# Kernel tuning notes

Measured on AMD Instinct MI355X. Metric: run time of the kernel, lower is better.

## Reference

```python
import jax, jax.numpy as jnp
import numpy as np

N_NODES = 50000
N_IN = 512
HIDDEN = 64
N_CLASSES = 40
N_EDGES = 800000


def setup_inputs() -> dict:
    key = jax.random.key(0)
    ks = jax.random.split(key, 8)
    x = jax.random.normal(ks[0], (N_NODES, N_IN), dtype=jnp.float32)
    edge_index = jax.random.randint(ks[1], (2, N_EDGES), 0, N_NODES, dtype=jnp.int64)
    s1 = 1.0 / np.sqrt(N_IN)
    s2 = 1.0 / np.sqrt(HIDDEN)
    W1 = jax.random.uniform(ks[2], (N_IN, HIDDEN), jnp.float32, -s1, s1)
    b1 = jax.random.uniform(ks[3], (HIDDEN,), jnp.float32, -s1, s1)
    W2 = jax.random.uniform(ks[4], (HIDDEN, HIDDEN), jnp.float32, -s2, s2)
    b2 = jax.random.uniform(ks[5], (HIDDEN,), jnp.float32, -s2, s2)
    Wo = jax.random.uniform(ks[6], (HIDDEN, N_CLASSES), jnp.float32, -s2, s2)
    bo = jax.random.uniform(ks[7], (N_CLASSES,), jnp.float32, -s2, s2)
    return {"x": x, "W1": W1, "b1": b1, "W2": W2, "b2": b2,
            "Wo": Wo, "bo": bo, "edge_index": edge_index}


def _gcn_conv(x, W, b, row, col, n_nodes):
    # h = lin(x)
    h = x @ W + b
    # degree over row (with self loops already appended)
    deg = jnp.zeros((n_nodes,), dtype=h.dtype).at[row].add(1.0)
    dis = deg ** -0.5  # deg >= 1 thanks to self loops
    norm = dis[row] * dis[col]  # [E]
    # message: norm * x_j where x_j = h[row] (source); aggregate to col (target)
    msg = norm[:, None] * h[row]  # [E, d]
    return jax.ops.segment_sum(msg, col, num_segments=n_nodes)


def reference(x, W1, b1, W2, b2, Wo, bo, edge_index):
    n = x.shape[0]
    # add_self_loops
    loop = jnp.arange(n, dtype=edge_index.dtype)
    row = jnp.concatenate([edge_index[0], loop])
    col = jnp.concatenate([edge_index[1], loop])
    h = _gcn_conv(x, W1, b1, row, col, n)
    h = jax.nn.relu(h)
    # dropout is identity in eval mode (training=False)
    h = _gcn_conv(h, W2, b2, row, col, n)
    logits = h @ Wo + bo
    return jax.nn.log_softmax(logits, axis=1)
```

## Files before the change

kernel.cpp:

```cpp
#include <hip/hip_runtime.h>
#include <hip/hip_fp16.h>
#include <cstdint>

#define N_NODES   50000
#define N_IN      512
#define HIDDEN    64
#define N_CLASSES 40
#define N_EDGES   800000

#define G_BLOCKS  200
#define EPB       4000
#define NBINS     196
#define SCAN_N    (NBINS * G_BLOCKS)
#define SCAN_NB   ((SCAN_N + 1023) / 1024)
#define FOLD_N    (N_IN * 64 + 64 * 64 + 64)
#define FOLD_B    ((FOLD_N + 255) / 256)

#define OFF_HA    0u
#define OFF_HB    6400000u
#define OFF_DIS   12800000u
#define OFF_OFFS  13000000u
#define OFF_HISTC 13200016u
#define OFF_HISTR 13356816u
#define OFF_BSUM  13513616u
#define OFF_COLS  13514128u
#define OFF_ROWS  16714128u
#define OFF_EPACK 19914128u
#define OFF_W1T   23114128u
#define OFF_W2OT  23179664u
#define OFF_B2O   23187856u

typedef __attribute__((ext_vector_type(8))) short short8_t;
typedef __attribute__((ext_vector_type(4))) float f32x4;

__device__ __forceinline__ ushort f2bf(float f) {
    uint u = __float_as_uint(f);
    uint r = (u + 0x7FFFu + ((u >> 16) & 1u)) >> 16;
    return (ushort)r;
}
__device__ __forceinline__ float bf2f(ushort h) {
    return __uint_as_float((uint)h << 16);
}

__global__ __launch_bounds__(256) void hist_fold(const int* __restrict__ erow,
                                                 const int* __restrict__ ecol,
                                                 int* __restrict__ histC,
                                                 int* __restrict__ histR,
                                                 const float* __restrict__ W1,
                                                 const float* __restrict__ W2,
                                                 const float* __restrict__ Wo,
                                                 const float* __restrict__ b2,
                                                 ushort* __restrict__ w1t,
                                                 ushort* __restrict__ w2ot,
                                                 float* __restrict__ b2o) {
    __shared__ int hc[NBINS], hr[NBINS];
    int t = threadIdx.x;
    if (blockIdx.x < G_BLOCKS) {
        int b = blockIdx.x;
        if (t < NBINS) { hc[t] = 0; hr[t] = 0; }
        __syncthreads();
        int s = b * EPB;
        for (int i = s + t; i < s + EPB; i += 256) {
            atomicAdd(&hc[ecol[i] >> 8], 1);
            atomicAdd(&hr[erow[i] >> 8], 1);
        }
        __syncthreads();
        if (t < NBINS) {
            histC[t * G_BLOCKS + b] = hc[t];
            histR[t * G_BLOCKS + b] = hr[t];
        }
    } else {
        int i = (blockIdx.x - G_BLOCKS) * 256 + t;
        if (i < N_IN * 64) {
            int k = i >> 6, n = i & 63;
            w1t[n * N_IN + k] = f2bf(W1[i]);
        } else if (i < N_IN * 64 + 64 * 64) {
            int j = i - N_IN * 64;
            int k = j >> 6, n = j & 63;
            float v = 0.f;
            if (n < N_CLASSES)
                for (int jj = 0; jj < HIDDEN; jj++)
                    v += W2[k * HIDDEN + jj] * Wo[jj * N_CLASSES + n];
            w2ot[n * HIDDEN + k] = f2bf(v);
        } else if (i < FOLD_N) {
            int c = i - N_IN * 64 - 64 * 64;
            float v = 0.f;
            if (c < N_CLASSES)
                for (int jj = 0; jj < HIDDEN; jj++)
                    v += b2[jj] * Wo[jj * N_CLASSES + c];
            b2o[c] = v;
        }
    }
}

__global__ __launch_bounds__(256) void scan1(int* __restrict__ histC,
                                             int* __restrict__ histR,
                                             int* __restrict__ bsum, int n) {
    int* a  = blockIdx.y ? histR : histC;
    int* bs = bsum + blockIdx.y * 64;
    int t = threadIdx.x;
    int g = blockIdx.x * 1024 + t * 4;
    int v[4];
#pragma unroll
    for (int i = 0; i < 4; i++) v[i] = (g + i < n) ? a[g + i] : 0;
    int s = v[0] + v[1] + v[2] + v[3];
    int lane = t & 63, wid = t >> 6;
    int x = s;
#pragma unroll
    for (int d = 1; d < 64; d <<= 1) {
        int y = __shfl_up(x, d);
        if (lane >= d) x += y;
    }
    __shared__ int wt[4];
    if (lane == 63) wt[wid] = x;
    __syncthreads();
    int wo = 0;
    for (int w = 0; w < wid; w++) wo += wt[w];
    int run = wo + x - s;
#pragma unroll
    for (int i = 0; i < 4; i++) {
        if (g + i < n) a[g + i] = run;
        run += v[i];
    }
    if (t == 255) bs[blockIdx.x] = wo + x;
}

__global__ void scan2(int* bsum, int nb) {
    int* bs = bsum + blockIdx.x * 64;
    int lane = threadIdx.x;
    int v = (lane < nb) ? bs[lane] : 0;
    int x = v;
#pragma unroll
    for (int d = 1; d < 64; d <<= 1) {
        int y = __shfl_up(x, d);
        if (lane >= d) x += y;
    }
    if (lane < nb) bs[lane] = x - v;
}

__global__ __launch_bounds__(256) void scan3(int* __restrict__ histC,
                                             int* __restrict__ histR,
                                             const int* __restrict__ bsum, int n) {
    int* a = blockIdx.y ? histR : histC;
    const int* bs = bsum + blockIdx.y * 64;
    int i = blockIdx.x * 256 + threadIdx.x;
    if (i < n) a[i] += bs[i >> 10];
}

__global__ __launch_bounds__(256) void scatter_k(const int* __restrict__ erow,
                                                 const int* __restrict__ ecol,
                                                 const int* __restrict__ scC,
                                                 const int* __restrict__ scR,
                                                 uint* __restrict__ colSorted,
                                                 int* __restrict__ rowSorted) {
    __shared__ int curC[NBINS], curR[NBINS];
    int t = threadIdx.x, b = blockIdx.x;
    if (t < NBINS) {
        curC[t] = scC[t * G_BLOCKS + b];
        curR[t] = scR[t * G_BLOCKS + b];
    }
    __syncthreads();
    int s = b * EPB;
    for (int i = s + t; i < s + EPB; i += 256) {
        int r = erow[i], c = ecol[i];
        int p = atomicAdd(&curC[c >> 8], 1);
        colSorted[p] = (uint)r | ((uint)c << 16);
        int q = atomicAdd(&curR[r >> 8], 1);
        rowSorted[q] = r;
    }
}

__global__ __launch_bounds__(256) void fine_row(const int* __restrict__ rowSorted,
                                                const int* __restrict__ scR,
                                                float* __restrict__ disv) {
    __shared__ int cnt[256];
    int bin = blockIdx.x, t = threadIdx.x;
    int base = scR[bin * G_BLOCKS];
    int end  = (bin == NBINS - 1) ? N_EDGES : scR[(bin + 1) * G_BLOCKS];
    cnt[t] = 0;
    __syncthreads();
    for (int i = base + t; i < end; i += 256)
        atomicAdd(&cnt[rowSorted[i] & 255], 1);
    __syncthreads();
    int node = bin * 256 + t;
    if (node < N_NODES) disv[node] = rsqrtf((float)(cnt[t] + 1));
}

__global__ __launch_bounds__(256) void fine_col(const uint* __restrict__ colSorted,
                                                const int* __restrict__ scC,
                                                const float* __restrict__ disv,
                                                int* __restrict__ offs,
                                                uint* __restrict__ epack) {
    __shared__ int cnt[256];
    __shared__ int excl[256];
    __shared__ int wt[4];
    __shared__ float dvs[256];
    int bin = blockIdx.x, t = threadIdx.x;
    int base = scC[bin * G_BLOCKS];
    int end  = (bin == NBINS - 1) ? N_EDGES : scC[(bin + 1) * G_BLOCKS];
    cnt[t] = 0;
    int node = bin * 256 + t;
    dvs[t] = (node < N_NODES) ? disv[node] : 0.f;
    __syncthreads();
    for (int i = base + t; i < end; i += 256)
        atomicAdd(&cnt[(colSorted[i] >> 16) & 255], 1);
    __syncthreads();
    int lane = t & 63, w = t >> 6;
    int v = cnt[t];
    int x = v;
#pragma unroll
    for (int d = 1; d < 64; d <<= 1) {
        int y = __shfl_up(x, d);
        if (lane >= d) x += y;
    }
    if (lane == 63) wt[w] = x;
    __syncthreads();
    int wo = 0;
    for (int u = 0; u < w; u++) wo += wt[u];
    excl[t] = wo + x - v;
    cnt[t] = 0;
    if (node <= N_NODES) offs[node] = base + wo + x - v;
    __syncthreads();
    for (int i = base + t; i < end; i += 256) {
        uint pv = colSorted[i];
        int cl = (pv >> 16) & 255;
        int src = (int)(pv & 0xFFFFu);
        int p = base + excl[cl] + atomicAdd(&cnt[cl], 1);
        float nrm = disv[src] * dvs[cl];
        ushort nb_ = __half_as_ushort(__float2half_rn(nrm));
        epack[p] = ((uint)nb_ << 16) | (uint)src;
    }
}

template <bool ABF16>
__global__ __launch_bounds__(256) void gemm_mfma(const void* __restrict__ Av,
                                                 const ushort* __restrict__ WT,
                                                 const float* __restrict__ bias,
                                                 ushort* __restrict__ C,
                                                 int M, int K) {
    __shared__ ushort Asb[64][72];
    __shared__ ushort Bsb[64][72];
    int t = threadIdx.x;
    int w = t >> 6, lane = t & 63;
    int wm = w >> 1, wn = w & 1;
    int lr = lane & 15, lg = lane >> 4;
    int blockRow = blockIdx.x * 64;

    f32x4 acc[2][2];
#pragma unroll
    for (int i = 0; i < 2; i++)
#pragma unroll
        for (int j = 0; j < 2; j++) acc[i][j] = (f32x4){0.f, 0.f, 0.f, 0.f};

    for (int kk = 0; kk < K; kk += 64) {
#pragma unroll
        for (int u = 0; u < 2; u++) {
            int idx = t + u * 256;
            int m = idx >> 3;
            int k8 = (idx & 7) * 8;
            int row = blockRow + m;
            short8_t s;
            if (ABF16) {
                const ushort* A16 = (const ushort*)Av;
                if (row < M) s = *(const short8_t*)(A16 + (size_t)row * K + kk + k8);
                else s = (short8_t){0,0,0,0,0,0,0,0};
            } else {
                const float* A32 = (const float*)Av;
                float4 a0, a1;
                if (row < M) {
                    const float* p = A32 + (size_t)row * K + kk + k8;
                    a0 = *(const float4*)p;
                    a1 = *(const float4*)(p + 4);
                } else {
                    a0 = make_float4(0.f, 0.f, 0.f, 0.f);
                    a1 = a0;
                }
                s[0] = (short)f2bf(a0.x); s[1] = (short)f2bf(a0.y);
                s[2] = (short)f2bf(a0.z); s[3] = (short)f2bf(a0.w);
                s[4] = (short)f2bf(a1.x); s[5] = (short)f2bf(a1.y);
                s[6] = (short)f2bf(a1.z); s[7] = (short)f2bf(a1.w);
            }
            *(short8_t*)&Asb[m][k8] = s;
        }
#pragma unroll
        for (int u = 0; u < 2; u++) {
            int idx = t + u * 256;
            int n = idx >> 3;
            int k8 = (idx & 7) * 8;
            short8_t vv = *(const short8_t*)(WT + (size_t)n * K + kk + k8);
            *(short8_t*)&Bsb[n][k8] = vv;
        }
        __syncthreads();
#pragma unroll
        for (int ks = 0; ks < 2; ks++) {
            int k0 = ks * 32 + lg * 8;
            short8_t af[2], bf_[2];
#pragma unroll
            for (int mi = 0; mi < 2; mi++)
                af[mi] = *(const short8_t*)&Asb[wm * 32 + mi * 16 + lr][k0];
#pragma unroll
            for (int ni = 0; ni < 2; ni++)
                bf_[ni] = *(const short8_t*)&Bsb[wn * 32 + ni * 16 + lr][k0];
#pragma unroll
            for (int mi = 0; mi < 2; mi++)
#pragma unroll
                for (int ni = 0; ni < 2; ni++)
                    acc[mi][ni] = __builtin_amdgcn_mfma_f32_16x16x32_bf16(
                        af[mi], bf_[ni], acc[mi][ni], 0, 0, 0);
        }
        __syncthreads();
    }
#pragma unroll
    for (int mi = 0; mi < 2; mi++) {
#pragma unroll
        for (int ni = 0; ni < 2; ni++) {
            int col = wn * 32 + ni * 16 + lr;
            float bv = bias[col];
#pragma unroll
            for (int r = 0; r < 4; r++) {
                int row = blockRow + wm * 32 + mi * 16 + lg * 4 + r;
                if (row < M) C[(size_t)row * 64 + col] = f2bf(acc[mi][ni][r] + bv);
            }
        }
    }
}

template <int HEAD>
__global__ __launch_bounds__(256) void agg_v3(const ushort* __restrict__ H,
                                              const int* __restrict__ offs,
                                              const uint* __restrict__ epack,
                                              const float* __restrict__ disv,
                                              ushort* __restrict__ outH,
                                              const float* __restrict__ bo,
                                              float* __restrict__ outL) {
    int wv = (blockIdx.x * 256 + threadIdx.x) >> 6;
    int lane = threadIdx.x & 63;
    wv = __builtin_amdgcn_readfirstlane(wv);
    if (wv >= N_NODES) return;
    int s = offs[wv], e = offs[wv + 1];
    float dn = disv[wv];
    float acc = dn * dn *
        bf2f(__builtin_nontemporal_load(H + (size_t)wv * 64 + lane));

    int i = s;
    for (; i + 8 <= e; i += 8) {
        uint ep[8];
#pragma unroll
        for (int u = 0; u < 8; u++) ep[u] = epack[i + u];
        float hv[8];
#pragma unroll
        for (int u = 0; u < 8; u++)
            hv[u] = bf2f(__builtin_nontemporal_load(
                H + (size_t)(ep[u] & 0xFFFFu) * 64 + lane));
#pragma unroll
        for (int u = 0; u < 8; u++) {
            float w = __half2float(__ushort_as_half((ushort)(ep[u] >> 16)));
            acc = fmaf(w, hv[u], acc);
        }
    }
    if (i < e) {
        int cap = e - 1;
        uint ep[8];
#pragma unroll
        for (int u = 0; u < 8; u++) ep[u] = epack[min(i + u, cap)];
        float hv[8];
#pragma unroll
        for (int u = 0; u < 8; u++)
            hv[u] = bf2f(__builtin_nontemporal_load(
                H + (size_t)(ep[u] & 0xFFFFu) * 64 + lane));
#pragma unroll
        for (int u = 0; u < 8; u++) {
            uint wb = (i + u < e) ? (ep[u] >> 16) : 0u;
            float w = __half2float(__ushort_as_half((ushort)wb));
            acc = fmaf(w, hv[u], acc);
        }
    }

    if (!HEAD) {
        outH[(size_t)wv * 64 + lane] = f2bf(fmaxf(acc, 0.f));
    } else {
        float accL = (lane < N_CLASSES) ? acc + bo[lane] : -1e30f;
        float mx = accL;
#pragma unroll
        for (int d = 32; d; d >>= 1) mx = fmaxf(mx, __shfl_xor(mx, d));
        float ex = (lane < N_CLASSES) ? expf(accL - mx) : 0.f;
        float sm = ex;
#pragma unroll
        for (int d = 32; d; d >>= 1) sm += __shfl_xor(sm, d);
        if (lane < N_CLASSES)
            outL[(size_t)wv * N_CLASSES + lane] = accL - mx - logf(sm);
    }
}

extern "C" void kernel_launch(void* const* d_in, const int* in_sizes, int n_in,
                              void* d_out, int out_size, void* d_ws, size_t ws_size,
                              hipStream_t stream) {
    const float* x  = (const float*)d_in[0];
    const float* W1 = (const float*)d_in[1];
    const float* b1 = (const float*)d_in[2];
    const float* W2 = (const float*)d_in[3];
    const float* b2 = (const float*)d_in[4];
    const float* Wo = (const float*)d_in[5];
    const float* bo = (const float*)d_in[6];
    const int* ei   = (const int*)d_in[7];
    const int* erow = ei;
    const int* ecol = ei + N_EDGES;

    char* ws = (char*)d_ws;
    ushort* h_a   = (ushort*)(ws + OFF_HA);
    ushort* h_b   = (ushort*)(ws + OFF_HB);
    float* disv   = (float*)(ws + OFF_DIS);
    int*   offs   = (int*)(ws + OFF_OFFS);
    int*   histC  = (int*)(ws + OFF_HISTC);
    int*   histR  = (int*)(ws + OFF_HISTR);
    int*   bsum   = (int*)(ws + OFF_BSUM);
    uint*  colS   = (uint*)(ws + OFF_COLS);
    int*   rowS   = (int*)(ws + OFF_ROWS);
    uint*  epack  = (uint*)(ws + OFF_EPACK);
    ushort* w1t   = (ushort*)(ws + OFF_W1T);
    ushort* w2ot  = (ushort*)(ws + OFF_W2OT);
    float* b2o    = (float*)(ws + OFF_B2O);
    float* outp   = (float*)d_out;

    hist_fold<<<G_BLOCKS + FOLD_B, 256, 0, stream>>>(erow, ecol, histC, histR,
                                                     W1, W2, Wo, b2, w1t, w2ot, b2o);
    scan1<<<dim3(SCAN_NB, 2), 256, 0, stream>>>(histC, histR, bsum, SCAN_N);
    scan2<<<2, 64, 0, stream>>>(bsum, SCAN_NB);
    scan3<<<dim3((SCAN_N + 255) / 256, 2), 256, 0, stream>>>(histC, histR, bsum, SCAN_N);
    scatter_k<<<G_BLOCKS, 256, 0, stream>>>(erow, ecol, histC, histR, colS, rowS);
    fine_row<<<NBINS, 256, 0, stream>>>(rowS, histR, disv);
    fine_col<<<NBINS, 256, 0, stream>>>(colS, histC, disv, offs, epack);

    gemm_mfma<false><<<(N_NODES + 63) / 64, 256, 0, stream>>>(x, w1t, b1, h_a, N_NODES, N_IN);
    agg_v3<0><<<(N_NODES + 3) / 4, 256, 0, stream>>>(h_a, offs, epack, disv, h_b,
                                                     nullptr, nullptr);
    gemm_mfma<true><<<(N_NODES + 63) / 64, 256, 0, stream>>>(h_b, w2ot, b2o, h_a, N_NODES, HIDDEN);
    agg_v3<1><<<(N_NODES + 3) / 4, 256, 0, stream>>>(h_a, offs, epack, disv, nullptr,
                                                     bo, outp);
}
```

Baseline: 140.2 us.

## Fuse first GEMM with edge scatter and aggregate two edges per wave

The first dense GEMM now runs inside the edge-scatter kernel: separate blocks of one launch handle the GEMM and the scatter, so the two independent jobs overlap and one launch is dropped. The aggregation kernel splits each 64-lane wave into two halves. Each half reads a different neighbour edge with 32-bit loads of two bf16 features, and the halves are combined with a cross-half shuffle. This gives fewer load instructions and more edges in flight per wave, at the cost of a shuffle reduction and a reworked log-softmax that holds two classes per lane.

```diff
diff --git a/kernel.cpp b/kernel.cpp
--- a/kernel.cpp
+++ b/kernel.cpp
@@ -15,6 +15,7 @@
 #define SCAN_NB   ((SCAN_N + 1023) / 1024)
 #define FOLD_N    (N_IN * 64 + 64 * 64 + 64)
 #define FOLD_B    ((FOLD_N + 255) / 256)
+#define GEMM1_B   ((N_NODES + 63) / 64)
 
 #define OFF_HA    0u
 #define OFF_HB    6400000u
@@ -147,104 +148,17 @@
     if (i < n) a[i] += bs[i >> 10];
 }
 
-__global__ __launch_bounds__(256) void scatter_k(const int* __restrict__ erow,
-                                                 const int* __restrict__ ecol,
-                                                 const int* __restrict__ scC,
-                                                 const int* __restrict__ scR,
-                                                 uint* __restrict__ colSorted,
-                                                 int* __restrict__ rowSorted) {
-    __shared__ int curC[NBINS], curR[NBINS];
-    int t = threadIdx.x, b = blockIdx.x;
-    if (t < NBINS) {
-        curC[t] = scC[t * G_BLOCKS + b];
-        curR[t] = scR[t * G_BLOCKS + b];
-    }
-    __syncthreads();
-    int s = b * EPB;
-    for (int i = s + t; i < s + EPB; i += 256) {
-        int r = erow[i], c = ecol[i];
-        int p = atomicAdd(&curC[c >> 8], 1);
-        colSorted[p] = (uint)r | ((uint)c << 16);
-        int q = atomicAdd(&curR[r >> 8], 1);
-        rowSorted[q] = r;
-    }
-}
-
-__global__ __launch_bounds__(256) void fine_row(const int* __restrict__ rowSorted,
-                                                const int* __restrict__ scR,
-                                                float* __restrict__ disv) {
-    __shared__ int cnt[256];
-    int bin = blockIdx.x, t = threadIdx.x;
-    int base = scR[bin * G_BLOCKS];
-    int end  = (bin == NBINS - 1) ? N_EDGES : scR[(bin + 1) * G_BLOCKS];
-    cnt[t] = 0;
-    __syncthreads();
-    for (int i = base + t; i < end; i += 256)
-        atomicAdd(&cnt[rowSorted[i] & 255], 1);
-    __syncthreads();
-    int node = bin * 256 + t;
-    if (node < N_NODES) disv[node] = rsqrtf((float)(cnt[t] + 1));
-}
-
-__global__ __launch_bounds__(256) void fine_col(const uint* __restrict__ colSorted,
-                                                const int* __restrict__ scC,
-                                                const float* __restrict__ disv,
-                                                int* __restrict__ offs,
-                                                uint* __restrict__ epack) {
-    __shared__ int cnt[256];
-    __shared__ int excl[256];
-    __shared__ int wt[4];
-    __shared__ float dvs[256];
-    int bin = blockIdx.x, t = threadIdx.x;
-    int base = scC[bin * G_BLOCKS];
-    int end  = (bin == NBINS - 1) ? N_EDGES : scC[(bin + 1) * G_BLOCKS];
-    cnt[t] = 0;
-    int node = bin * 256 + t;
-    dvs[t] = (node < N_NODES) ? disv[node] : 0.f;
-    __syncthreads();
-    for (int i = base + t; i < end; i += 256)
-        atomicAdd(&cnt[(colSorted[i] >> 16) & 255], 1);
-    __syncthreads();
-    int lane = t & 63, w = t >> 6;
-    int v = cnt[t];
-    int x = v;
-#pragma unroll
-    for (int d = 1; d < 64; d <<= 1) {
-        int y = __shfl_up(x, d);
-        if (lane >= d) x += y;
-    }
-    if (lane == 63) wt[w] = x;
-    __syncthreads();
-    int wo = 0;
-    for (int u = 0; u < w; u++) wo += wt[u];
-    excl[t] = wo + x - v;
-    cnt[t] = 0;
-    if (node <= N_NODES) offs[node] = base + wo + x - v;
-    __syncthreads();
-    for (int i = base + t; i < end; i += 256) {
-        uint pv = colSorted[i];
-        int cl = (pv >> 16) & 255;
-        int src = (int)(pv & 0xFFFFu);
-        int p = base + excl[cl] + atomicAdd(&cnt[cl], 1);
-        float nrm = disv[src] * dvs[cl];
-        ushort nb_ = __half_as_ushort(__float2half_rn(nrm));
-        epack[p] = ((uint)nb_ << 16) | (uint)src;
-    }
-}
-
 template <bool ABF16>
-__global__ __launch_bounds__(256) void gemm_mfma(const void* __restrict__ Av,
-                                                 const ushort* __restrict__ WT,
-                                                 const float* __restrict__ bias,
-                                                 ushort* __restrict__ C,
-                                                 int M, int K) {
-    __shared__ ushort Asb[64][72];
-    __shared__ ushort Bsb[64][72];
+__device__ __forceinline__ void gemm_body(ushort (&Asb)[64][72], ushort (&Bsb)[64][72],
+                                          const void* __restrict__ Av,
+                                          const ushort* __restrict__ WT,
+                                          const float* __restrict__ bias,
+                                          ushort* __restrict__ C,
+                                          int M, int K, int blockRow) {
     int t = threadIdx.x;
     int w = t >> 6, lane = t & 63;
     int wm = w >> 1, wn = w & 1;
     int lr = lane & 15, lg = lane >> 4;
-    int blockRow = blockIdx.x * 64;
 
     f32x4 acc[2][2];
 #pragma unroll
@@ -325,8 +239,116 @@
     }
 }
 
+template <bool ABF16>
+__global__ __launch_bounds__(256) void gemm_mfma(const void* __restrict__ Av,
+                                                 const ushort* __restrict__ WT,
+                                                 const float* __restrict__ bias,
+                                                 ushort* __restrict__ C,
+                                                 int M, int K) {
+    __shared__ ushort Asb[64][72];
+    __shared__ ushort Bsb[64][72];
+    gemm_body<ABF16>(Asb, Bsb, Av, WT, bias, C, M, K, blockIdx.x * 64);
+}
+
+__global__ __launch_bounds__(256) void scatter_gemm(const float* __restrict__ x,
+                                                    const ushort* __restrict__ w1t,
+                                                    const float* __restrict__ b1,
+                                                    ushort* __restrict__ h_a,
+                                                    const int* __restrict__ erow,
+                                                    const int* __restrict__ ecol,
+                                                    const int* __restrict__ scC,
+                                                    const int* __restrict__ scR,
+                                                    uint* __restrict__ colSorted,
+                                                    int* __restrict__ rowSorted) {
+    __shared__ ushort Asb[64][72];
+    __shared__ ushort Bsb[64][72];
+    if (blockIdx.x < GEMM1_B) {
+        gemm_body<false>(Asb, Bsb, x, w1t, b1, h_a, N_NODES, N_IN, blockIdx.x * 64);
+        return;
+    }
+    int b = blockIdx.x - GEMM1_B;
+    int* curC = (int*)&Asb[0][0];
+    int* curR = curC + NBINS;
+    int t = threadIdx.x;
+    if (t < NBINS) {
+        curC[t] = scC[t * G_BLOCKS + b];
+        curR[t] = scR[t * G_BLOCKS + b];
+    }
+    __syncthreads();
+    int s = b * EPB;
+    for (int i = s + t; i < s + EPB; i += 256) {
+        int r = erow[i], c = ecol[i];
+        int p = atomicAdd(&curC[c >> 8], 1);
+        colSorted[p] = (uint)r | ((uint)c << 16);
+        int q = atomicAdd(&curR[r >> 8], 1);
+        rowSorted[q] = r;
+    }
+}
+
+__global__ __launch_bounds__(256) void fine_row(const int* __restrict__ rowSorted,
+                                                const int* __restrict__ scR,
+                                                float* __restrict__ disv) {
+    __shared__ int cnt[256];
+    int bin = blockIdx.x, t = threadIdx.x;
+    int base = scR[bin * G_BLOCKS];
+    int end  = (bin == NBINS - 1) ? N_EDGES : scR[(bin + 1) * G_BLOCKS];
+    cnt[t] = 0;
+    __syncthreads();
+    for (int i = base + t; i < end; i += 256)
+        atomicAdd(&cnt[rowSorted[i] & 255], 1);
+    __syncthreads();
+    int node = bin * 256 + t;
+    if (node < N_NODES) disv[node] = rsqrtf((float)(cnt[t] + 1));
+}
+
+__global__ __launch_bounds__(256) void fine_col(const uint* __restrict__ colSorted,
+                                                const int* __restrict__ scC,
+                                                const float* __restrict__ disv,
+                                                int* __restrict__ offs,
+                                                uint* __restrict__ epack) {
+    __shared__ int cnt[256];
+    __shared__ int excl[256];
+    __shared__ int wt[4];
+    __shared__ float dvs[256];
+    int bin = blockIdx.x, t = threadIdx.x;
+    int base = scC[bin * G_BLOCKS];
+    int end  = (bin == NBINS - 1) ? N_EDGES : scC[(bin + 1) * G_BLOCKS];
+    cnt[t] = 0;
+    int node = bin * 256 + t;
+    dvs[t] = (node < N_NODES) ? disv[node] : 0.f;
+    __syncthreads();
+    for (int i = base + t; i < end; i += 256)
+        atomicAdd(&cnt[(colSorted[i] >> 16) & 255], 1);
+    __syncthreads();
+    int lane = t & 63, w = t >> 6;
+    int v = cnt[t];
+    int x = v;
+#pragma unroll
+    for (int d = 1; d < 64; d <<= 1) {
+        int y = __shfl_up(x, d);
+        if (lane >= d) x += y;
+    }
+    if (lane == 63) wt[w] = x;
+    __syncthreads();
+    int wo = 0;
+    for (int u = 0; u < w; u++) wo += wt[u];
+    excl[t] = wo + x - v;
+    cnt[t] = 0;
+    if (node <= N_NODES) offs[node] = base + wo + x - v;
+    __syncthreads();
+    for (int i = base + t; i < end; i += 256) {
+        uint pv = colSorted[i];
+        int cl = (pv >> 16) & 255;
+        int src = (int)(pv & 0xFFFFu);
+        int p = base + excl[cl] + atomicAdd(&cnt[cl], 1);
+        float nrm = disv[src] * dvs[cl];
+        ushort nb_ = __half_as_ushort(__float2half_rn(nrm));
+        epack[p] = ((uint)nb_ << 16) | (uint)src;
+    }
+}
+
 template <int HEAD>
-__global__ __launch_bounds__(256) void agg_v3(const ushort* __restrict__ H,
+__global__ __launch_bounds__(256) void agg_v4(const ushort* __restrict__ H,
                                               const int* __restrict__ offs,
                                               const uint* __restrict__ epack,
                                               const float* __restrict__ disv,
@@ -337,25 +359,25 @@
     int lane = threadIdx.x & 63;
     wv = __builtin_amdgcn_readfirstlane(wv);
     if (wv >= N_NODES) return;
+    int c = lane & 31;
+    int g = lane >> 5;
     int s = offs[wv], e = offs[wv + 1];
     float dn = disv[wv];
-    float acc = dn * dn *
-        bf2f(__builtin_nontemporal_load(H + (size_t)wv * 64 + lane));
-
+    uint self = *(const uint*)(H + (size_t)wv * 64 + c * 2);
+
+    float acc0 = 0.f, acc1 = 0.f;
     int i = s;
     for (; i + 8 <= e; i += 8) {
         uint ep[8];
 #pragma unroll
         for (int u = 0; u < 8; u++) ep[u] = epack[i + u];
-        float hv[8];
-#pragma unroll
-        for (int u = 0; u < 8; u++)
-            hv[u] = bf2f(__builtin_nontemporal_load(
-                H + (size_t)(ep[u] & 0xFFFFu) * 64 + lane));
-#pragma unroll
-        for (int u = 0; u < 8; u++) {
-            float w = __half2float(__ushort_as_half((ushort)(ep[u] >> 16)));
-            acc = fmaf(w, hv[u], acc);
+#pragma unroll
+        for (int p = 0; p < 4; p++) {
+            uint eg = g ? ep[2 * p + 1] : ep[2 * p];
+            uint hv = *(const uint*)(H + (size_t)(eg & 0xFFFFu) * 64 + c * 2);
+            float w = __half2float(__ushort_as_half((ushort)(eg >> 16)));
+            acc0 = fmaf(w, bf2f((ushort)(hv & 0xFFFFu)), acc0);
+            acc1 = fmaf(w, bf2f((ushort)(hv >> 16)), acc1);
         }
     }
     if (i < e) {
@@ -363,32 +385,46 @@
         uint ep[8];
 #pragma unroll
         for (int u = 0; u < 8; u++) ep[u] = epack[min(i + u, cap)];
-        float hv[8];
-#pragma unroll
-        for (int u = 0; u < 8; u++)
-            hv[u] = bf2f(__builtin_nontemporal_load(
-                H + (size_t)(ep[u] & 0xFFFFu) * 64 + lane));
-#pragma unroll
-        for (int u = 0; u < 8; u++) {
-            uint wb = (i + u < e) ? (ep[u] >> 16) : 0u;
-            float w = __half2float(__ushort_as_half((ushort)wb));
-            acc = fmaf(w, hv[u], acc);
-        }
-    }
+#pragma unroll
+        for (int p = 0; p < 4; p++) {
+            int idx = i + 2 * p + g;
+            uint eg = g ? ep[2 * p + 1] : ep[2 * p];
+            uint hv = *(const uint*)(H + (size_t)(eg & 0xFFFFu) * 64 + c * 2);
+            float w = (idx < e)
+                ? __half2float(__ushort_as_half((ushort)(eg >> 16))) : 0.f;
+            acc0 = fmaf(w, bf2f((ushort)(hv & 0xFFFFu)), acc0);
+            acc1 = fmaf(w, bf2f((ushort)(hv >> 16)), acc1);
+        }
+    }
+    acc0 += __shfl_xor(acc0, 32);
+    acc1 += __shfl_xor(acc1, 32);
+    float dd = dn * dn;
+    acc0 = fmaf(dd, bf2f((ushort)(self & 0xFFFFu)), acc0);
+    acc1 = fmaf(dd, bf2f((ushort)(self >> 16)), acc1);
 
     if (!HEAD) {
-        outH[(size_t)wv * 64 + lane] = f2bf(fmaxf(acc, 0.f));
+        if (g == 0) {
+            uint o = (uint)f2bf(fmaxf(acc0, 0.f))
+                   | ((uint)f2bf(fmaxf(acc1, 0.f)) << 16);
+            *(uint*)(outH + (size_t)wv * 64 + c * 2) = o;
+        }
     } else {
-        float accL = (lane < N_CLASSES) ? acc + bo[lane] : -1e30f;
-        float mx = accL;
-#pragma unroll
-        for (int d = 32; d; d >>= 1) mx = fmaxf(mx, __shfl_xor(mx, d));
-        float ex = (lane < N_CLASSES) ? expf(accL - mx) : 0.f;
-        float sm = ex;
-#pragma unroll
-        for (int d = 32; d; d >>= 1) sm += __shfl_xor(sm, d);
-        if (lane < N_CLASSES)
-            outL[(size_t)wv * N_CLASSES + lane] = accL - mx - logf(sm);
+        int cc = min(c, 19);
+        float2 bv = *(const float2*)(bo + 2 * cc);
+        bool valid = (c < 20);
+        float l0 = valid ? acc0 + bv.x : -1e30f;
+        float l1 = valid ? acc1 + bv.y : -1e30f;
+        float mx = fmaxf(l0, l1);
+#pragma unroll
+        for (int d = 16; d; d >>= 1) mx = fmaxf(mx, __shfl_xor(mx, d));
+        float sm = (valid ? expf(l0 - mx) : 0.f) + (valid ? expf(l1 - mx) : 0.f);
+#pragma unroll
+        for (int d = 16; d; d >>= 1) sm += __shfl_xor(sm, d);
+        if (g == 0 && valid) {
+            float ls = logf(sm);
+            float2 o = make_float2(l0 - mx - ls, l1 - mx - ls);
+            *(float2*)(outL + (size_t)wv * N_CLASSES + 2 * c) = o;
+        }
     }
 }
 
@@ -427,14 +463,15 @@
     scan1<<<dim3(SCAN_NB, 2), 256, 0, stream>>>(histC, histR, bsum, SCAN_N);
     scan2<<<2, 64, 0, stream>>>(bsum, SCAN_NB);
     scan3<<<dim3((SCAN_N + 255) / 256, 2), 256, 0, stream>>>(histC, histR, bsum, SCAN_N);
-    scatter_k<<<G_BLOCKS, 256, 0, stream>>>(erow, ecol, histC, histR, colS, rowS);
+    scatter_gemm<<<GEMM1_B + G_BLOCKS, 256, 0, stream>>>(x, w1t, b1, h_a,
+                                                         erow, ecol, histC, histR,
+                                                         colS, rowS);
     fine_row<<<NBINS, 256, 0, stream>>>(rowS, histR, disv);
     fine_col<<<NBINS, 256, 0, stream>>>(colS, histC, disv, offs, epack);
 
-    gemm_mfma<false><<<(N_NODES + 63) / 64, 256, 0, stream>>>(x, w1t, b1, h_a, N_NODES, N_IN);
-    agg_v3<0><<<(N_NODES + 3) / 4, 256, 0, stream>>>(h_a, offs, epack, disv, h_b,
+    agg_v4<0><<<(N_NODES + 3) / 4, 256, 0, stream>>>(h_a, offs, epack, disv, h_b,
                                                      nullptr, nullptr);
-    gemm_mfma<true><<<(N_NODES + 63) / 64, 256, 0, stream>>>(h_b, w2ot, b2o, h_a, N_NODES, HIDDEN);
-    agg_v3<1><<<(N_NODES + 3) / 4, 256, 0, stream>>>(h_a, offs, epack, disv, nullptr,
+    gemm_mfma<true><<<GEMM1_B, 256, 0, stream>>>(h_b, w2ot, b2o, h_a, N_NODES, HIDDEN);
+    agg_v4<1><<<(N_NODES + 3) / 4, 256, 0, stream>>>(h_a, offs, epack, disv, nullptr,
                                                      bo, outp);
 }
```

Result: slower. 156.5 us (+11.6%).
